# Kernel tuning notes

Measured on AMD Instinct MI355X. Metric: run time of the kernel, lower is better.

## Reference

```python
import jax, jax.numpy as jnp
import numpy as np

B, K, NP = 2, 48, 25            # batch, context_length, grid_x*grid_y
C, H, L = 768, 12, 6            # n_embd, n_head, n_layer
COLORS, VOCAB, IS = 10, 40, 26  # color_num, vocab_size, intention_size
MAXT = 1000                     # max_timestep
TOK = NP + 4                    # tokens per timestep (rtg, 25 states, action, pnp, intention)
T = K * TOK                     # total sequence length


def layernorm(x, g, b, eps=1e-5):
    m = x.mean(-1, keepdims=True)
    v = ((x - m) ** 2).mean(-1, keepdims=True)
    return (x - m) * jax.lax.rsqrt(v + eps) * g + b


def causal_attn(x, wq, bq, wk, bk, wv, bv, wo, bo):
    Bx, Tx, Cx = x.shape
    hd = Cx // H
    def heads(w, bb):
        return (x @ w + bb).reshape(Bx, Tx, H, hd).transpose(0, 2, 1, 3)
    q, k, v = heads(wq, bq), heads(wk, bk), heads(wv, bv)
    att = jnp.einsum('bhqd,bhkd->bhqk', q, k) * (1.0 / np.sqrt(hd))
    mask = jnp.tril(jnp.ones((Tx, Tx), bool))
    att = jnp.where(mask, att, -jnp.inf)
    att = jax.nn.softmax(att, axis=-1)
    y = jnp.einsum('bhqk,bhkd->bhqd', att, v).transpose(0, 2, 1, 3).reshape(Bx, Tx, Cx)
    return y @ wo + bo


def setup_inputs() -> dict:
    key = jax.random.key(0)
    ks = iter(jax.random.split(key, 64))
    def nrm(shape):
        return jax.random.normal(next(ks), shape, jnp.float32) * 0.02
    inp = dict(
        states=jax.random.randint(next(ks), (B, K * NP), 0, COLORS),
        actions=jax.random.randint(next(ks), (B, K), 0, VOCAB),
        rtgs=jax.random.normal(next(ks), (B, K), jnp.float32),
        timesteps=jax.random.randint(next(ks), (B, K), 0, MAXT + 1),
        pnp=jax.random.normal(next(ks), (B, K, NP), jnp.float32),
        intentions=jax.random.randint(next(ks), (B, K, 2), 0, IS),
        pos_emb=nrm((K + 1, C)),               # (block_size, C)
        global_pos_emb=nrm((MAXT + 1, C)),
        state_tab=nrm((COLORS, C)),
        action_tab=nrm((VOCAB, C)),
        ret_W=nrm((1, C)), ret_b=jnp.zeros((C,)),
        pnp_W=nrm((NP, C)), pnp_b=jnp.zeros((C,)),
        src_tab=nrm((IS, C)), dst_tab=nrm((IS, C)),
        int_W=nrm((2 * C, C)), int_b=jnp.zeros((C,)),
        ln1_g=jnp.ones((L, C)), ln1_b=jnp.zeros((L, C)),
        ln2_g=jnp.ones((L, C)), ln2_b=jnp.zeros((L, C)),
        Wq=nrm((L, C, C)), bq=jnp.zeros((L, C)),
        Wk=nrm((L, C, C)), bk=jnp.zeros((L, C)),
        Wv=nrm((L, C, C)), bv=jnp.zeros((L, C)),
        Wo=nrm((L, C, C)), bo=jnp.zeros((L, C)),
        Wm1=nrm((L, C, 4 * C)), bm1=jnp.zeros((L, 4 * C)),
        Wm2=nrm((L, 4 * C, C)), bm2=jnp.zeros((L, C)),
        lnf_g=jnp.ones((C,)), lnf_b=jnp.zeros((C,)),
        Whs=nrm((C, COLORS)), bhs=jnp.zeros((COLORS,)),
        Wha=nrm((C, VOCAB)), bha=jnp.zeros((VOCAB,)),
        Whr=nrm((C, 1)), bhr=jnp.zeros((1,)),
        Whi=nrm((C, 2 * IS)), bhi=jnp.zeros((2 * IS,)),
    )
    return inp


def reference(states, actions, rtgs, timesteps, pnp, intentions,
              pos_emb, global_pos_emb, state_tab, action_tab,
              ret_W, ret_b, pnp_W, pnp_b, src_tab, dst_tab, int_W, int_b,
              ln1_g, ln1_b, ln2_g, ln2_b, Wq, bq, Wk, bk, Wv, bv, Wo, bo,
              Wm1, bm1, Wm2, bm2, lnf_g, lnf_b,
              Whs, bhs, Wha, bha, Whr, bhr, Whi, bhi):
    # --- embeddings, interleaved as [rtg, state_0..24, action, pnp, intention] per timestep ---
    st = state_tab[states].reshape(B, K, NP, C)                    # strided writes 1+i::TOK
    ae = action_tab[actions][:, :, None, :]
    re = (rtgs[..., None] @ ret_W + ret_b)[:, :, None, :]          # rtgs.unsqueeze(-1) -> Linear(1,C)
    pe = (pnp @ pnp_W + pnp_b)[:, :, None, :]
    ie_in = jnp.concatenate([src_tab[intentions[..., 0]], dst_tab[intentions[..., 1]]], axis=-1)
    ie = (ie_in @ int_W + int_b)[:, :, None, :]
    tok = jnp.concatenate([re, st, ae, pe, ie], axis=2).reshape(B, T, C)
    # --- positions: gather global + local pos_emb[:block_size-1], repeat_interleave by TOK ---
    pos = global_pos_emb[timesteps] + pos_emb[:K][None]            # (B, K, C)
    x = tok + jnp.repeat(pos, TOK, axis=1)
    # --- transformer stack (dropout p=0) ---
    def blk(h, p):
        l1g, l1b, l2g, l2b, wq, bq_, wk, bk_, wv, bv_, wo, bo_, w1, b1, w2, b2 = p
        h = h + causal_attn(layernorm(h, l1g, l1b), wq, bq_, wk, bk_, wv, bv_, wo, bo_)
        m = layernorm(h, l2g, l2b)
        h = h + jax.nn.gelu(m @ w1 + b1, approximate=False) @ w2 + b2
        return h, None
    x, _ = jax.lax.scan(blk, x, (ln1_g, ln1_b, ln2_g, ln2_b, Wq, bq, Wk, bk, Wv, bv, Wo, bo, Wm1, bm1, Wm2, bm2))
    x = layernorm(x, lnf_g, lnf_b)
    xr = x.reshape(B, K, TOK, C)
    logits = x @ Whs + bhs                                         # (B, T, COLORS)
    logit_action = xr[:, :, NP + 1] @ Wha + bha                    # (B, K, VOCAB)
    logit_rtg = (xr[:, :, 0] @ Whr + bhr)[..., 0]                  # (B, K)
    li = xr[:, :, NP + 3] @ Whi + bhi                              # (B, K, 2*IS)
    return logits, logit_action, logit_rtg, li[..., :IS], li[..., IS:]
```

## Files before the change

### kernel.cpp

```cpp
#include <hip/hip_runtime.h>
#include <hip/hip_bf16.h>
#include <math.h>


typedef __hip_bfloat16 bf16;
typedef __attribute__((ext_vector_type(4))) short s4v;
typedef __attribute__((ext_vector_type(8))) short s8v;
typedef __attribute__((ext_vector_type(4))) float f4v;
typedef unsigned int u32;

#define DEV static __device__ __forceinline__

constexpr int NBATCH = 2;
constexpr int NK   = 48;
constexpr int NNP  = 25;
constexpr int NC   = 768;
constexpr int NH   = 12;
constexpr int NL   = 6;
constexpr int NTOK = 29;
constexpr int NT   = NK * NTOK;
constexpr int NM   = NBATCH * NT;
constexpr int MPAD = 2816;

DEV float bs2f(short s) {
  unsigned u = ((unsigned)(unsigned short)s) << 16;
  float f; __builtin_memcpy(&f, &u, 4); return f;
}
DEV short f2bs(float f) {
  bf16 h = __float2bfloat16(f);
  short s; __builtin_memcpy(&s, &h, 2); return s;
}

DEV void async16(const short* g, short* l) {
  __builtin_amdgcn_global_load_lds(
      (const __attribute__((address_space(1))) u32*)g,
      (__attribute__((address_space(3))) u32*)l, 16, 0, 0);
}

__global__ __launch_bounds__(256) void transpose_kernel(
    const float* __restrict__ src, bf16* __restrict__ dst, int R, int C)
{
  int c0 = blockIdx.x * 32, r0 = blockIdx.y * 32;
  __shared__ float tl[32][33];
  int rr = threadIdx.x >> 5, cc = threadIdx.x & 31;
#pragma unroll
  for (int p = 0; p < 4; p++)
    tl[rr + p * 8][cc] = src[(long)(r0 + rr + p * 8) * C + c0 + cc];
  __syncthreads();
#pragma unroll
  for (int p = 0; p < 4; p++)
    dst[(long)(c0 + rr + p * 8) * R + r0 + cc] = __float2bfloat16(tl[cc][rr + p * 8]);
}

__global__ __launch_bounds__(256) void transpose_layer_kernel(
    const float* __restrict__ Wq, const float* __restrict__ Wk,
    const float* __restrict__ Wv, const float* __restrict__ Wo,
    const float* __restrict__ Wm1, const float* __restrict__ Wm2,
    bf16* __restrict__ WqkvT, bf16* __restrict__ WoT,
    bf16* __restrict__ Wm1T, bf16* __restrict__ Wm2T, int multi)
{
  int blk = blockIdx.x;
  int l = blk / 864, t = blk - l * 864;
  long so = (long)l * 768 * 768;
  long mo = (long)l * 768 * 3072;
  long dl = multi ? l : 0;
  const float* src; bf16* dst; int R, C, tile;
  if (t < 216) {
    int m = t / 72; tile = t - m * 72;
    src = (m == 0 ? Wq : (m == 1 ? Wk : Wv)) + so;
    dst = WqkvT + dl * (2304L * 768) + (long)m * 768 * 768; R = 768; C = 768;
  } else if (t < 288)  { src = Wo + so;  dst = WoT  + dl * (768L * 768);  tile = t - 216; R = 768;  C = 768;  }
  else if (t < 576)    { src = Wm1 + mo; dst = Wm1T + dl * (3072L * 768); tile = t - 288; R = 768;  C = 3072; }
  else                 { src = Wm2 + mo; dst = Wm2T + dl * (768L * 3072); tile = t - 576; R = 3072; C = 768;  }
  int ct = C / 64;
  int tr = tile / ct, tc = tile - tr * ct;
  int r0 = tr * 128, c0 = tc * 64;

  __shared__ short tl[128][66];
  int cg = threadIdx.x & 15, rg = threadIdx.x >> 4;
#pragma unroll
  for (int p = 0; p < 8; p++) {
    int row = rg + p * 16;
    f4v v = *(const f4v*)(src + (long)(r0 + row) * C + c0 + cg * 4);
    tl[row][cg * 4 + 0] = f2bs(v.x);
    tl[row][cg * 4 + 1] = f2bs(v.y);
    tl[row][cg * 4 + 2] = f2bs(v.z);
    tl[row][cg * 4 + 3] = f2bs(v.w);
  }
  __syncthreads();
#pragma unroll
  for (int p = 0; p < 4; p++) {
    int d = rg + p * 16;
    const short* base = &tl[cg * 8][d];
    s8v w;
    w.s0 = base[0 * 66]; w.s1 = base[1 * 66]; w.s2 = base[2 * 66]; w.s3 = base[3 * 66];
    w.s4 = base[4 * 66]; w.s5 = base[5 * 66]; w.s6 = base[6 * 66]; w.s7 = base[7 * 66];
    *(s8v*)((short*)dst + (long)(c0 + d) * R + r0 + cg * 8) = w;
  }
}

__global__ __launch_bounds__(256) void gather_ie_kernel(
    const int* __restrict__ intentions, const float* __restrict__ src_tab,
    const float* __restrict__ dst_tab, bf16* __restrict__ ie_in)
{
  int idx = blockIdx.x * 256 + threadIdx.x;
  if (idx >= 96 * 1536) return;
  int row = idx / 1536, col = idx - row * 1536;
  float v;
  if (col < 768) v = src_tab[intentions[row * 2 + 0] * 768 + col];
  else           v = dst_tab[intentions[row * 2 + 1] * 768 + col - 768];
  ie_in[idx] = __float2bfloat16(v);
}

__global__ __launch_bounds__(256) void embed_kernel(
    const int* __restrict__ states, const int* __restrict__ actions,
    const float* __restrict__ rtgs, const int* __restrict__ timesteps,
    const float* __restrict__ pnp,
    const float* __restrict__ pos_emb, const float* __restrict__ gpe,
    const float* __restrict__ state_tab, const float* __restrict__ action_tab,
    const float* __restrict__ retW, const float* __restrict__ retb,
    const float* __restrict__ pnpW, const float* __restrict__ pnpb,
    const bf16* __restrict__ ieb, float* __restrict__ X)
{
  int bk = blockIdx.x;
  int b = bk / NK, ts = bk - b * NK;
  int c = blockIdx.y * 256 + threadIdx.x;

  float rtg = rtgs[bk];
  int tstep = timesteps[bk];
  int act   = actions[bk];

  long base = (long)(b * NT + ts * NTOK) * NC;
  float pos = gpe[(long)tstep * NC + c] + pos_emb[ts * NC + c];

  X[base + c] = rtg * retW[c] + retb[c] + pos;
  const int* sp = states + bk * NNP;
#pragma unroll
  for (int i = 0; i < NNP; i++)
    X[base + (1 + i) * NC + c] = state_tab[sp[i] * NC + c] + pos;
  X[base + 26 * NC + c] = action_tab[act * NC + c] + pos;
  float ap = pnpb[c];
  const float* pv = pnp + bk * NNP;
#pragma unroll
  for (int i = 0; i < NNP; i++) ap += pv[i] * pnpW[i * NC + c];
  X[base + 27 * NC + c] = ap + pos;
  X[base + 28 * NC + c] = __bfloat162float(ieb[bk * NC + c]) + pos;
}

__global__ __launch_bounds__(256) void ln_kernel(
    const float* __restrict__ X, bf16* __restrict__ XN,
    const float* __restrict__ g, const float* __restrict__ bt)
{
  int row = blockIdx.x * 4 + (threadIdx.x >> 6);
  int lane = threadIdx.x & 63;
  const float* x = X + (long)row * NC;
  f4v v0 = *(const f4v*)(x + lane * 4);
  f4v v1 = *(const f4v*)(x + 256 + lane * 4);
  f4v v2 = *(const f4v*)(x + 512 + lane * 4);
  float s = v0.x + v0.y + v0.z + v0.w + v1.x + v1.y + v1.z + v1.w
          + v2.x + v2.y + v2.z + v2.w;
#pragma unroll
  for (int o = 32; o > 0; o >>= 1) s += __shfl_xor(s, o);
  float mean = s * (1.0f / NC);
  f4v d0, d1, d2;
  d0.x = v0.x - mean; d0.y = v0.y - mean; d0.z = v0.z - mean; d0.w = v0.w - mean;
  d1.x = v1.x - mean; d1.y = v1.y - mean; d1.z = v1.z - mean; d1.w = v1.w - mean;
  d2.x = v2.x - mean; d2.y = v2.y - mean; d2.z = v2.z - mean; d2.w = v2.w - mean;
  float qq = d0.x*d0.x + d0.y*d0.y + d0.z*d0.z + d0.w*d0.w
           + d1.x*d1.x + d1.y*d1.y + d1.z*d1.z + d1.w*d1.w
           + d2.x*d2.x + d2.y*d2.y + d2.z*d2.z + d2.w*d2.w;
#pragma unroll
  for (int o = 32; o > 0; o >>= 1) qq += __shfl_xor(qq, o);
  float var = qq * (1.0f / NC);
  float rs = 1.0f / sqrtf(var + 1e-5f);
  short* xn = (short*)XN + (long)row * NC;
  f4v g0 = *(const f4v*)(g + lane * 4);
  f4v g1 = *(const f4v*)(g + 256 + lane * 4);
  f4v g2 = *(const f4v*)(g + 512 + lane * 4);
  f4v b0 = *(const f4v*)(bt + lane * 4);
  f4v b1 = *(const f4v*)(bt + 256 + lane * 4);
  f4v b2 = *(const f4v*)(bt + 512 + lane * 4);
  s4v w0, w1, w2;
  w0.x = f2bs(d0.x * rs * g0.x + b0.x); w0.y = f2bs(d0.y * rs * g0.y + b0.y);
  w0.z = f2bs(d0.z * rs * g0.z + b0.z); w0.w = f2bs(d0.w * rs * g0.w + b0.w);
  w1.x = f2bs(d1.x * rs * g1.x + b1.x); w1.y = f2bs(d1.y * rs * g1.y + b1.y);
  w1.z = f2bs(d1.z * rs * g1.z + b1.z); w1.w = f2bs(d1.w * rs * g1.w + b1.w);
  w2.x = f2bs(d2.x * rs * g2.x + b2.x); w2.y = f2bs(d2.y * rs * g2.y + b2.y);
  w2.z = f2bs(d2.z * rs * g2.z + b2.z); w2.w = f2bs(d2.w * rs * g2.w + b2.w);
  *(s4v*)(xn + lane * 4)       = w0;
  *(s4v*)(xn + 256 + lane * 4) = w1;
  *(s4v*)(xn + 512 + lane * 4) = w2;
}

template<int BM, int BN>
__global__ __launch_bounds__(256) void gemm_kernel(
    const bf16* __restrict__ A, const bf16* __restrict__ WT,
    const float* __restrict__ b0, const float* __restrict__ b1,
    const float* __restrict__ b2, int Nsplit,
    bf16* __restrict__ outb, float* __restrict__ resid,
    int M, int N, int K, int flags)
{
  constexpr int IM  = BM / 64;
  constexpr int JN  = BN / 16;
  constexpr int ACH = BM / 64;
  constexpr int BCH = BN / 64;
  __shared__ __align__(1024) short As[2][BM * 32];
  __shared__ __align__(1024) short Bs[2][BN * 32];

  int tid = threadIdx.x, wave = tid >> 6, lane = tid & 63;
  int quad = lane >> 4, l16 = lane & 15;
  int m0 = blockIdx.y * BM, n0 = blockIdx.x * BN;
  int wm = wave * (BM / 4);
  int lr = lane >> 2, lc = (lane & 3) * 8;

  const short* Ag = (const short*)A + (long)m0 * K + lc;
  const short* Bg = (const short*)WT + (long)n0 * K + lc;

  const short* ag[ACH]; int alo[ACH];
#pragma unroll
  for (int c = 0; c < ACH; c++) {
    int rbase = wave * (16 * ACH) + c * 16;
    ag[c] = Ag + (long)(rbase + lr) * K;
    alo[c] = rbase * 32;
  }
  const short* bg[BCH]; int blo[BCH];
#pragma unroll
  for (int c = 0; c < BCH; c++) {
    int rbase = wave * (16 * BCH) + c * 16;
    bg[c] = Bg + (long)(rbase + lr) * K;
    blo[c] = rbase * 32;
  }

  f4v zero4 = {0.f, 0.f, 0.f, 0.f};
  f4v acc[IM][JN];
#pragma unroll
  for (int i = 0; i < IM; i++)
#pragma unroll
    for (int j = 0; j < JN; j++) acc[i][j] = zero4;

  int nk = K >> 5;
#pragma unroll
  for (int c = 0; c < ACH; c++) async16(ag[c], &As[0][alo[c]]);
#pragma unroll
  for (int c = 0; c < BCH; c++) async16(bg[c], &Bs[0][blo[c]]);
  __syncthreads();

  for (int kt = 0; kt < nk; kt++) {
    int cur = kt & 1, nxt = cur ^ 1;
    if (kt + 1 < nk) {
      int ko = (kt + 1) << 5;
#pragma unroll
      for (int c = 0; c < ACH; c++) async16(ag[c] + ko, &As[nxt][alo[c]]);
#pragma unroll
      for (int c = 0; c < BCH; c++) async16(bg[c] + ko, &Bs[nxt][blo[c]]);
    }
    s8v af[IM], bf8[JN];
#pragma unroll
    for (int i = 0; i < IM; i++) {
      const short* p = &As[cur][(wm + i * 16 + l16) * 32 + quad * 8];
      af[i].lo = *(const s4v*)p; af[i].hi = *(const s4v*)(p + 4);
    }
#pragma unroll
    for (int j = 0; j < JN; j++) {
      const short* p = &Bs[cur][(j * 16 + l16) * 32 + quad * 8];
      bf8[j].lo = *(const s4v*)p; bf8[j].hi = *(const s4v*)(p + 4);
    }
#pragma unroll
    for (int i = 0; i < IM; i++)
#pragma unroll
      for (int j = 0; j < JN; j++)
        acc[i][j] = __builtin_amdgcn_mfma_f32_16x16x32_bf16(af[i], bf8[j], acc[i][j], 0, 0, 0);
    __syncthreads();
  }

#pragma unroll
  for (int i = 0; i < IM; i++) {
    int rbase = m0 + wm + i * 16 + quad * 4;
#pragma unroll
    for (int j = 0; j < JN; j++) {
      int bc = n0 + j * 16;
      int wsel = bc / Nsplit;
      const float* bp = wsel == 0 ? b0 : (wsel == 1 ? b1 : b2);
      float bv = bp[bc - wsel * Nsplit + l16];
      int col = bc + l16;
#pragma unroll
      for (int r = 0; r < 4; r++) {
        int row = rbase + r;
        if (row < M) {
          float v = acc[i][j][r] + bv;
          if (flags & 1) v = 0.5f * v * (1.0f + erff(v * 0.70710678118654752f));
          if (flags & 2) resid[(long)row * N + col] += v;
          else outb[(long)row * N + col] = __float2bfloat16(v);
        }
      }
    }
  }
}

constexpr int ASTR = 72;

__global__ __launch_bounds__(256) void attn_kernel(
    const bf16* __restrict__ QKV, bf16* __restrict__ Yg)
{
  int qt = blockIdx.x, h = blockIdx.y, b = blockIdx.z;
  int q0 = qt * 64;
  int tid = threadIdx.x, wave = tid >> 6, lane = tid & 63, quad = lane >> 4, l16 = lane & 15;

  __shared__ short Qs[64 * ASTR];
  __shared__ short Ks[64 * ASTR];
  __shared__ short Vt[64 * ASTR];
  __shared__ short Ps[64 * ASTR];

  int r = tid >> 2, c16 = (tid & 3) * 16;
  const short* src = (const short*)QKV;
  s8v zz = {0,0,0,0,0,0,0,0};

  s8v qv0 = zz, qv1 = zz;
  if (q0 + r < NT) {
    const s8v* p = (const s8v*)(src + (long)(b * NT + q0 + r) * 2304 + h * 64 + c16);
    qv0 = p[0]; qv1 = p[1];
  }
  {
    short* qp = &Qs[r * ASTR + c16];
    *(s4v*)(qp    ) = qv0.lo; *(s4v*)(qp + 4) = qv0.hi;
    *(s4v*)(qp + 8) = qv1.lo; *(s4v*)(qp + 12) = qv1.hi;
  }

  f4v zero4 = {0.f, 0.f, 0.f, 0.f};
  f4v Of[4];
#pragma unroll
  for (int j = 0; j < 4; j++) Of[j] = zero4;
  float m_r[4], l_r[4];
#pragma unroll
  for (int rg = 0; rg < 4; rg++) { m_r[rg] = -1e30f; l_r[rg] = 0.f; }

  int kend = q0 + 63; if (kend > NT - 1) kend = NT - 1;

  s8v kv0 = zz, kv1 = zz, vv0 = zz, vv1 = zz;
  if (r < NT) {
    const s8v* pk = (const s8v*)(src + (long)(b * NT + r) * 2304 + 768 + h * 64 + c16);
    kv0 = pk[0]; kv1 = pk[1];
    const s8v* pvv = (const s8v*)(src + (long)(b * NT + r) * 2304 + 1536 + h * 64 + c16);
    vv0 = pvv[0]; vv1 = pvv[1];
  }

  for (int k0 = 0; k0 <= kend; k0 += 64) {
    __syncthreads();
    {
      short* kp = &Ks[r * ASTR + c16];
      *(s4v*)(kp    ) = kv0.lo; *(s4v*)(kp + 4) = kv0.hi;
      *(s4v*)(kp + 8) = kv1.lo; *(s4v*)(kp + 12) = kv1.hi;
      short* vt = &Vt[c16 * ASTR + r];
      vt[ 0 * ASTR] = vv0.s0; vt[ 1 * ASTR] = vv0.s1; vt[ 2 * ASTR] = vv0.s2; vt[ 3 * ASTR] = vv0.s3;
      vt[ 4 * ASTR] = vv0.s4; vt[ 5 * ASTR] = vv0.s5; vt[ 6 * ASTR] = vv0.s6; vt[ 7 * ASTR] = vv0.s7;
      vt[ 8 * ASTR] = vv1.s0; vt[ 9 * ASTR] = vv1.s1; vt[10 * ASTR] = vv1.s2; vt[11 * ASTR] = vv1.s3;
      vt[12 * ASTR] = vv1.s4; vt[13 * ASTR] = vv1.s5; vt[14 * ASTR] = vv1.s6; vt[15 * ASTR] = vv1.s7;
    }
    __syncthreads();

    int k1 = k0 + 64;
    s8v nk0 = zz, nk1 = zz, nv0 = zz, nv1 = zz;
    if (k1 <= kend && k1 + r < NT) {
      const s8v* pk = (const s8v*)(src + (long)(b * NT + k1 + r) * 2304 + 768 + h * 64 + c16);
      nk0 = pk[0]; nk1 = pk[1];
      const s8v* pvv = (const s8v*)(src + (long)(b * NT + k1 + r) * 2304 + 1536 + h * 64 + c16);
      nv0 = pvv[0]; nv1 = pvv[1];
    }

    f4v sa[4];
#pragma unroll
    for (int j = 0; j < 4; j++) sa[j] = zero4;
#pragma unroll
    for (int ks = 0; ks < 2; ks++) {
      const short* pa = &Qs[(wave * 16 + l16) * ASTR + ks * 32 + quad * 8];
      s8v aq; aq.lo = *(const s4v*)pa; aq.hi = *(const s4v*)(pa + 4);
#pragma unroll
      for (int j = 0; j < 4; j++) {
        const short* pb = &Ks[(j * 16 + l16) * ASTR + ks * 32 + quad * 8];
        s8v bk8; bk8.lo = *(const s4v*)pb; bk8.hi = *(const s4v*)(pb + 4);
        sa[j] = __builtin_amdgcn_mfma_f32_16x16x32_bf16(aq, bk8, sa[j], 0, 0, 0);
      }
    }

#pragma unroll
    for (int j = 0; j < 4; j++) {
#pragma unroll
      for (int rg = 0; rg < 4; rg++) {
        int gq = q0 + wave * 16 + quad * 4 + rg;
        int gk = k0 + j * 16 + l16;
        sa[j][rg] = (gk <= gq && gq < NT) ? sa[j][rg] * 0.125f : -1e30f;
      }
    }

#pragma unroll
    for (int rg = 0; rg < 4; rg++) {
      float mx = fmaxf(fmaxf(sa[0][rg], sa[1][rg]), fmaxf(sa[2][rg], sa[3][rg]));
      mx = fmaxf(mx, __shfl_xor(mx, 1));
      mx = fmaxf(mx, __shfl_xor(mx, 2));
      mx = fmaxf(mx, __shfl_xor(mx, 4));
      mx = fmaxf(mx, __shfl_xor(mx, 8));
      float mn = fmaxf(m_r[rg], mx);
      float al = __expf(m_r[rg] - mn);
      m_r[rg] = mn;
      float ps = 0.f;
#pragma unroll
      for (int j = 0; j < 4; j++) {
        float e = __expf(sa[j][rg] - mn);
        sa[j][rg] = e;
        ps += e;
      }
      ps += __shfl_xor(ps, 1);
      ps += __shfl_xor(ps, 2);
      ps += __shfl_xor(ps, 4);
      ps += __shfl_xor(ps, 8);
      l_r[rg] = l_r[rg] * al + ps;
#pragma unroll
      for (int j = 0; j < 4; j++) Of[j][rg] *= al;
    }

#pragma unroll
    for (int j = 0; j < 4; j++)
#pragma unroll
      for (int rg = 0; rg < 4; rg++)
        Ps[(wave * 16 + quad * 4 + rg) * ASTR + j * 16 + l16] = f2bs(sa[j][rg]);
    __syncthreads();

#pragma unroll
    for (int ks = 0; ks < 2; ks++) {
      const short* pa = &Ps[(wave * 16 + l16) * ASTR + ks * 32 + quad * 8];
      s8v ap8; ap8.lo = *(const s4v*)pa; ap8.hi = *(const s4v*)(pa + 4);
#pragma unroll
      for (int j = 0; j < 4; j++) {
        const short* pb = &Vt[(j * 16 + l16) * ASTR + ks * 32 + quad * 8];
        s8v vp8; vp8.lo = *(const s4v*)pb; vp8.hi = *(const s4v*)(pb + 4);
        Of[j] = __builtin_amdgcn_mfma_f32_16x16x32_bf16(ap8, vp8, Of[j], 0, 0, 0);
      }
    }

    kv0 = nk0; kv1 = nk1; vv0 = nv0; vv1 = nv1;
  }

#pragma unroll
  for (int rg = 0; rg < 4; rg++) {
    int rloc = wave * 16 + quad * 4 + rg;
    int gq = q0 + rloc;
    if (gq < NT) {
      float inv = 1.0f / l_r[rg];
#pragma unroll
      for (int j = 0; j < 4; j++) {
        float ov = Of[j][rg] * inv;
        Yg[(long)(b * NT + gq) * NC + h * 64 + j * 16 + l16] = __float2bfloat16(ov);
      }
    }
  }
}

__global__ __launch_bounds__(256) void head_kernel(
    const bf16* __restrict__ XN, const float* __restrict__ Whs,
    const float* __restrict__ bhs,
    const float* __restrict__ Wha, const float* __restrict__ bha,
    const float* __restrict__ Whr, const float* __restrict__ bhr,
    const float* __restrict__ Whi, const float* __restrict__ bhi,
    float* __restrict__ out0, float* __restrict__ outA,
    float* __restrict__ outR, float* __restrict__ outS,
    float* __restrict__ outD)
{
  int tid = threadIdx.x;
  const short* xs = (const short*)XN;
  if (blockIdx.x < 109) {
    int idx = blockIdx.x * 256 + tid;
    if (idx >= NM * 10) return;
    int row = idx / 10, n = idx - row * 10;
    const short* x = xs + (long)row * NC;
    float a0 = bhs[n], a1 = 0.f, a2 = 0.f, a3 = 0.f;
    for (int k = 0; k < NC; k += 4) {
      a0 += bs2f(x[k    ]) * Whs[(k    ) * 10 + n];
      a1 += bs2f(x[k + 1]) * Whs[(k + 1) * 10 + n];
      a2 += bs2f(x[k + 2]) * Whs[(k + 2) * 10 + n];
      a3 += bs2f(x[k + 3]) * Whs[(k + 3) * 10 + n];
    }
    out0[idx] = a0 + a1 + a2 + a3;
    return;
  }
  int blk = blockIdx.x - 109;
  int b = blk / NK, ts = blk - b * NK;
  if (tid >= 93) return;
  if (tid < 40) {
    long row = (long)(b * NT + ts * NTOK + 26) * NC;
    float a0 = bha[tid], a1 = 0.f, a2 = 0.f, a3 = 0.f;
    for (int k = 0; k < NC; k += 4) {
      a0 += bs2f(xs[row + k    ]) * Wha[(k    ) * 40 + tid];
      a1 += bs2f(xs[row + k + 1]) * Wha[(k + 1) * 40 + tid];
      a2 += bs2f(xs[row + k + 2]) * Wha[(k + 2) * 40 + tid];
      a3 += bs2f(xs[row + k + 3]) * Wha[(k + 3) * 40 + tid];
    }
    outA[blk * 40 + tid] = a0 + a1 + a2 + a3;
  } else if (tid == 40) {
    long row = (long)(b * NT + ts * NTOK) * NC;
    float a0 = bhr[0], a1 = 0.f, a2 = 0.f, a3 = 0.f;
    for (int k = 0; k < NC; k += 4) {
      a0 += bs2f(xs[row + k    ]) * Whr[k    ];
      a1 += bs2f(xs[row + k + 1]) * Whr[k + 1];
      a2 += bs2f(xs[row + k + 2]) * Whr[k + 2];
      a3 += bs2f(xs[row + k + 3]) * Whr[k + 3];
    }
    outR[blk] = a0 + a1 + a2 + a3;
  } else {
    int n = tid - 41;
    long row = (long)(b * NT + ts * NTOK + 28) * NC;
    float a0 = bhi[n], a1 = 0.f, a2 = 0.f, a3 = 0.f;
    for (int k = 0; k < NC; k += 4) {
      a0 += bs2f(xs[row + k    ]) * Whi[(k    ) * 52 + n];
      a1 += bs2f(xs[row + k + 1]) * Whi[(k + 1) * 52 + n];
      a2 += bs2f(xs[row + k + 2]) * Whi[(k + 2) * 52 + n];
      a3 += bs2f(xs[row + k + 3]) * Whi[(k + 3) * 52 + n];
    }
    if (n < 26) outS[blk * 26 + n] = a0 + a1 + a2 + a3;
    else        outD[blk * 26 + (n - 26)] = a0 + a1 + a2 + a3;
  }
}

extern "C" void kernel_launch(void* const* d_in, const int* in_sizes, int n_in,
                              void* d_out, int out_size, void* d_ws, size_t ws_size,
                              hipStream_t stream)
{
  (void)in_sizes; (void)n_in; (void)out_size;

  const int*   states     = (const int*)  d_in[0];
  const int*   actions    = (const int*)  d_in[1];
  const float* rtgs       = (const float*)d_in[2];
  const int*   timesteps  = (const int*)  d_in[3];
  const float* pnp        = (const float*)d_in[4];
  const int*   intentions = (const int*)  d_in[5];
  const float* pos_emb    = (const float*)d_in[6];
  const float* gpe        = (const float*)d_in[7];
  const float* state_tab  = (const float*)d_in[8];
  const float* action_tab = (const float*)d_in[9];
  const float* retW  = (const float*)d_in[10];
  const float* retb  = (const float*)d_in[11];
  const float* pnpW  = (const float*)d_in[12];
  const float* pnpb  = (const float*)d_in[13];
  const float* src_tab = (const float*)d_in[14];
  const float* dst_tab = (const float*)d_in[15];
  const float* intW  = (const float*)d_in[16];
  const float* intb  = (const float*)d_in[17];
  const float* ln1g  = (const float*)d_in[18];
  const float* ln1b  = (const float*)d_in[19];
  const float* ln2g  = (const float*)d_in[20];
  const float* ln2b  = (const float*)d_in[21];
  const float* Wq = (const float*)d_in[22];
  const float* bq = (const float*)d_in[23];
  const float* Wk = (const float*)d_in[24];
  const float* bk = (const float*)d_in[25];
  const float* Wv = (const float*)d_in[26];
  const float* bv = (const float*)d_in[27];
  const float* Wo = (const float*)d_in[28];
  const float* bo = (const float*)d_in[29];
  const float* Wm1 = (const float*)d_in[30];
  const float* bm1 = (const float*)d_in[31];
  const float* Wm2 = (const float*)d_in[32];
  const float* bm2 = (const float*)d_in[33];
  const float* lnfg = (const float*)d_in[34];
  const float* lnfb = (const float*)d_in[35];
  const float* Whs = (const float*)d_in[36];
  const float* bhs = (const float*)d_in[37];
  const float* Wha = (const float*)d_in[38];
  const float* bha = (const float*)d_in[39];
  const float* Whr = (const float*)d_in[40];
  const float* bhr = (const float*)d_in[41];
  const float* Whi = (const float*)d_in[42];
  const float* bhi = (const float*)d_in[43];

  char* wsb = (char*)d_ws;
  float* X   = (float*)(wsb);
  bf16* XN   = (bf16*)(wsb + 8650752);
  bf16* QKVb = (bf16*)(wsb + 12976128);
  bf16* Yb   = (bf16*)(wsb + 25952256);
  bf16* H1   = QKVb;
  bf16* WTbase = (bf16*)(wsb + 30277632);

  const size_t NEED_BIG = 30277632UL + 84934656UL + 2949120UL;
  bool big = ws_size >= NEED_BIG;

  long sQKV = 2304L * 768, sO = 768L * 768, sM1 = 3072L * 768, sM2 = 768L * 3072;
  bf16 *WqkvT, *WoT, *Wm1T, *Wm2T, *intWT;
  if (big) {
    WqkvT = WTbase;
    WoT   = WqkvT + 6 * sQKV;
    Wm1T  = WoT   + 6 * sO;
    Wm2T  = Wm1T  + 6 * sM1;
    intWT = Wm2T  + 6 * sM2;
  } else {
    WqkvT = WTbase;
    WoT   = WqkvT + sQKV;
    Wm1T  = WoT + sO;
    Wm2T  = Wm1T + sM1;
    intWT = WTbase;
  }
  bf16* ie_in = intWT + 768L * 1536;
  bf16* ieb   = ie_in + 128L * 1536;

  float* out0 = (float*)d_out;
  float* out1 = out0 + 27840;
  float* out2 = out1 + 3840;
  float* out3 = out2 + 96;
  float* out4 = out3 + 2496;

  transpose_kernel<<<dim3(24, 48), 256, 0, stream>>>(intW, intWT, 1536, 768);
  gather_ie_kernel<<<(96 * 1536 + 255) / 256, 256, 0, stream>>>(intentions, src_tab, dst_tab, ie_in);
  gemm_kernel<64, 64><<<dim3(12, 2), 256, 0, stream>>>(ie_in, intWT, intb, intb, intb, 768,
      ieb, nullptr, 96, 768, 1536, 0);
  embed_kernel<<<dim3(96, 3), 256, 0, stream>>>(
      states, actions, rtgs, timesteps, pnp, pos_emb, gpe, state_tab, action_tab,
      retW, retb, pnpW, pnpb, ieb, X);

  if (big)
    transpose_layer_kernel<<<864 * NL, 256, 0, stream>>>(
        Wq, Wk, Wv, Wo, Wm1, Wm2, WqkvT, WoT, Wm1T, Wm2T, 1);

  for (int l = 0; l < NL; l++) {
    const long wofs = (long)l * NC * NC;
    const long mofs = (long)l * NC * 4 * NC;
    if (!big)
      transpose_layer_kernel<<<864, 256, 0, stream>>>(
          Wq + wofs, Wk + wofs, Wv + wofs, Wo + wofs, Wm1 + mofs, Wm2 + mofs,
          WqkvT, WoT, Wm1T, Wm2T, 0);
    bf16* wqkv = big ? WqkvT + l * sQKV : WqkvT;
    bf16* wo   = big ? WoT   + l * sO   : WoT;
    bf16* wm1  = big ? Wm1T  + l * sM1  : Wm1T;
    bf16* wm2  = big ? Wm2T  + l * sM2  : Wm2T;

    ln_kernel<<<NM / 4, 256, 0, stream>>>(X, XN, ln1g + l * NC, ln1b + l * NC);
    gemm_kernel<128, 64><<<dim3(36, 22), 256, 0, stream>>>(XN, wqkv,
        bq + l * NC, bk + l * NC, bv + l * NC, 768, QKVb, nullptr, NM, 2304, NC, 0);
    attn_kernel<<<dim3(22, NH, NBATCH), 256, 0, stream>>>(QKVb, Yb);
    gemm_kernel<64, 64><<<dim3(12, 44), 256, 0, stream>>>(Yb, wo,
        bo + l * NC, bo + l * NC, bo + l * NC, 768, nullptr, X, NM, 768, NC, 2);
    ln_kernel<<<NM / 4, 256, 0, stream>>>(X, XN, ln2g + l * NC, ln2b + l * NC);
    gemm_kernel<128, 64><<<dim3(48, 22), 256, 0, stream>>>(XN, wm1,
        bm1 + l * 4 * NC, bm1 + l * 4 * NC, bm1 + l * 4 * NC, 4 * NC, H1, nullptr,
        NM, 3072, NC, 1);
    gemm_kernel<64, 64><<<dim3(12, 44), 256, 0, stream>>>(H1, wm2,
        bm2 + l * NC, bm2 + l * NC, bm2 + l * NC, 768, nullptr, X, NM, 768, 4 * NC, 2);
  }
  ln_kernel<<<NM / 4, 256, 0, stream>>>(X, XN, lnfg, lnfb);
  head_kernel<<<109 + NBATCH * NK, 256, 0, stream>>>(XN, Whs, bhs, Wha, bha,
      Whr, bhr, Whi, bhi, out0, out1, out2, out3, out4);
}
```

Baseline: 1.589 ms.

## Use 2x2 wave tiling for QKV/MLP1 GEMMs and split-K for MLP2

Generalizes the GEMM kernel to a configurable wave grid (WM x WN) and an optional split-K along a third grid dimension. QKV and MLP-up GEMMs move to 128x128 tiles with 2x2 waves, raising reuse per block and halving block count. The MLP-down GEMM (K=3072) is split in two along K and accumulates into the residual with atomic adds, adding parallelism at the cost of atomic traffic and nondeterministic summation order.

```diff
diff --git a/kernel.cpp b/kernel.cpp
--- a/kernel.cpp
+++ b/kernel.cpp
@@ -192,7 +192,7 @@
   *(s4v*)(xn + 512 + lane * 4) = w2;
 }
 
-template<int BM, int BN>
+template<int BM, int BN, int WM, int WN, int KSPLIT = 1>
 __global__ __launch_bounds__(256) void gemm_kernel(
     const bf16* __restrict__ A, const bf16* __restrict__ WT,
     const float* __restrict__ b0, const float* __restrict__ b1,
@@ -200,8 +200,8 @@
     bf16* __restrict__ outb, float* __restrict__ resid,
     int M, int N, int K, int flags)
 {
-  constexpr int IM  = BM / 64;
-  constexpr int JN  = BN / 16;
+  constexpr int IM  = BM / (WM * 16);
+  constexpr int JN  = BN / (WN * 16);
   constexpr int ACH = BM / 64;
   constexpr int BCH = BN / 64;
   __shared__ __align__(1024) short As[2][BM * 32];
@@ -210,11 +210,15 @@
   int tid = threadIdx.x, wave = tid >> 6, lane = tid & 63;
   int quad = lane >> 4, l16 = lane & 15;
   int m0 = blockIdx.y * BM, n0 = blockIdx.x * BN;
-  int wm = wave * (BM / 4);
+  int wm = (wave / WN) * (IM * 16);
+  int wn = (wave % WN) * (JN * 16);
   int lr = lane >> 2, lc = (lane & 3) * 8;
 
-  const short* Ag = (const short*)A + (long)m0 * K + lc;
-  const short* Bg = (const short*)WT + (long)n0 * K + lc;
+  int kbeg = (KSPLIT > 1) ? blockIdx.z * (K / KSPLIT) : 0;
+  int kl = K / KSPLIT;
+
+  const short* Ag = (const short*)A + (long)m0 * K + kbeg + lc;
+  const short* Bg = (const short*)WT + (long)n0 * K + kbeg + lc;
 
   const short* ag[ACH]; int alo[ACH];
 #pragma unroll
@@ -238,7 +242,7 @@
 #pragma unroll
     for (int j = 0; j < JN; j++) acc[i][j] = zero4;
 
-  int nk = K >> 5;
+  int nk = kl >> 5;
 #pragma unroll
   for (int c = 0; c < ACH; c++) async16(ag[c], &As[0][alo[c]]);
 #pragma unroll
@@ -262,7 +266,7 @@
     }
 #pragma unroll
     for (int j = 0; j < JN; j++) {
-      const short* p = &Bs[cur][(j * 16 + l16) * 32 + quad * 8];
+      const short* p = &Bs[cur][(wn + j * 16 + l16) * 32 + quad * 8];
       bf8[j].lo = *(const s4v*)p; bf8[j].hi = *(const s4v*)(p + 4);
     }
 #pragma unroll
@@ -273,15 +277,16 @@
     __syncthreads();
   }
 
+  bool addb = (KSPLIT == 1) || (blockIdx.z == 0);
 #pragma unroll
   for (int i = 0; i < IM; i++) {
     int rbase = m0 + wm + i * 16 + quad * 4;
 #pragma unroll
     for (int j = 0; j < JN; j++) {
-      int bc = n0 + j * 16;
+      int bc = n0 + wn + j * 16;
       int wsel = bc / Nsplit;
       const float* bp = wsel == 0 ? b0 : (wsel == 1 ? b1 : b2);
-      float bv = bp[bc - wsel * Nsplit + l16];
+      float bv = addb ? bp[bc - wsel * Nsplit + l16] : 0.f;
       int col = bc + l16;
 #pragma unroll
       for (int r = 0; r < 4; r++) {
@@ -289,8 +294,10 @@
         if (row < M) {
           float v = acc[i][j][r] + bv;
           if (flags & 1) v = 0.5f * v * (1.0f + erff(v * 0.70710678118654752f));
-          if (flags & 2) resid[(long)row * N + col] += v;
-          else outb[(long)row * N + col] = __float2bfloat16(v);
+          if (flags & 2) {
+            if (KSPLIT > 1) atomicAdd(&resid[(long)row * N + col], v);
+            else            resid[(long)row * N + col] += v;
+          } else outb[(long)row * N + col] = __float2bfloat16(v);
         }
       }
     }
@@ -608,7 +615,7 @@
 
   transpose_kernel<<<dim3(24, 48), 256, 0, stream>>>(intW, intWT, 1536, 768);
   gather_ie_kernel<<<(96 * 1536 + 255) / 256, 256, 0, stream>>>(intentions, src_tab, dst_tab, ie_in);
-  gemm_kernel<64, 64><<<dim3(12, 2), 256, 0, stream>>>(ie_in, intWT, intb, intb, intb, 768,
+  gemm_kernel<64, 64, 4, 1><<<dim3(12, 2), 256, 0, stream>>>(ie_in, intWT, intb, intb, intb, 768,
       ieb, nullptr, 96, 768, 1536, 0);
   embed_kernel<<<dim3(96, 3), 256, 0, stream>>>(
       states, actions, rtgs, timesteps, pnp, pos_emb, gpe, state_tab, action_tab,
@@ -631,16 +638,16 @@
     bf16* wm2  = big ? Wm2T  + l * sM2  : Wm2T;
 
     ln_kernel<<<NM / 4, 256, 0, stream>>>(X, XN, ln1g + l * NC, ln1b + l * NC);
-    gemm_kernel<128, 64><<<dim3(36, 22), 256, 0, stream>>>(XN, wqkv,
+    gemm_kernel<128, 128, 2, 2><<<dim3(18, 22), 256, 0, stream>>>(XN, wqkv,
         bq + l * NC, bk + l * NC, bv + l * NC, 768, QKVb, nullptr, NM, 2304, NC, 0);
     attn_kernel<<<dim3(22, NH, NBATCH), 256, 0, stream>>>(QKVb, Yb);
-    gemm_kernel<64, 64><<<dim3(12, 44), 256, 0, stream>>>(Yb, wo,
+    gemm_kernel<64, 64, 4, 1><<<dim3(12, 44), 256, 0, stream>>>(Yb, wo,
         bo + l * NC, bo + l * NC, bo + l * NC, 768, nullptr, X, NM, 768, NC, 2);
     ln_kernel<<<NM / 4, 256, 0, stream>>>(X, XN, ln2g + l * NC, ln2b + l * NC);
-    gemm_kernel<128, 64><<<dim3(48, 22), 256, 0, stream>>>(XN, wm1,
+    gemm_kernel<128, 128, 2, 2><<<dim3(24, 22), 256, 0, stream>>>(XN, wm1,
         bm1 + l * 4 * NC, bm1 + l * 4 * NC, bm1 + l * 4 * NC, 4 * NC, H1, nullptr,
         NM, 3072, NC, 1);
-    gemm_kernel<64, 64><<<dim3(12, 44), 256, 0, stream>>>(H1, wm2,
+    gemm_kernel<64, 64, 4, 1, 2><<<dim3(12, 44, 2), 256, 0, stream>>>(H1, wm2,
         bm2 + l * NC, bm2 + l * NC, bm2 + l * NC, 768, nullptr, X, NM, 768, 4 * NC, 2);
   }
   ln_kernel<<<NM / 4, 256, 0, stream>>>(X, XN, lnfg, lnfb);
```

After: 1.557 ms. 1.02x faster.
